# Performance work log

Measured on AMD Instinct MI355X. Metric: run time of the kernel, lower is better.

The kernel has to match this reference:

```python
import jax, jax.numpy as jnp
import numpy as np
from jax import lax

B = 256
R_ITERS = 3

def squash(x):
    # x * |x| / (1 + |x|^2), applied along last axis
    n = jnp.linalg.norm(x, axis=-1, keepdims=True)
    return x * n / (1.0 + n * n)

def conv2d(x, w, b, stride):
    y = lax.conv_general_dilated(x, w, window_strides=(stride, stride), padding='VALID',
                                 dimension_numbers=('NCHW', 'OIHW', 'NCHW'))
    return y + b[None, :, None, None]

def setup_inputs() -> dict:
    key = jax.random.key(0)
    ks = jax.random.split(key, 12)
    s = 0.05
    return {
        'x': jax.random.normal(ks[0], (B, 1, 28, 28), jnp.float32),
        'label': jax.random.randint(ks[1], (B,), 0, 10),
        'conv1_w': jax.random.normal(ks[2], (256, 1, 9, 9), jnp.float32) * s,
        'conv1_b': jnp.zeros((256,), jnp.float32),
        'pconv_w': jax.random.normal(ks[3], (256, 256, 9, 9), jnp.float32) * s,
        'pconv_b': jnp.zeros((256,), jnp.float32),
        'W_dig': jax.random.normal(ks[4], (1152, 10, 16, 8), jnp.float32),
        'dec_w1': jax.random.normal(ks[5], (512, 160), jnp.float32) * s,
        'dec_b1': jnp.zeros((512,), jnp.float32),
        'dec_w2': jax.random.normal(ks[6], (1024, 512), jnp.float32) * s,
        'dec_b2': jnp.zeros((1024,), jnp.float32),
        'dec_w3': jax.random.normal(ks[7], (784, 1024), jnp.float32) * s,
        'dec_b3': jnp.zeros((784,), jnp.float32),
    }

def reference(x, label, conv1_w, conv1_b, pconv_w, pconv_b, W_dig,
              dec_w1, dec_b1, dec_w2, dec_b2, dec_w3, dec_b3):
    # conv stem: [B,1,28,28] -> [B,256,20,20]
    h = conv2d(x, conv1_w, conv1_b, 1)
    # primary caps conv: -> [B,256,6,6] -> [B,1152,8] -> squash
    h = conv2d(h, pconv_w, pconv_b, 2)
    caps = squash(h.reshape(h.shape[0], -1, 8))
    # prediction vectors u_hat: [B, 1152, 10, 16]
    u = jnp.einsum('iond,bid->bion', W_dig, caps)
    # dynamic routing (softmax over input-capsule axis, per original code)
    b = jnp.zeros_like(u)
    for r in range(1, R_ITERS + 1):
        c = jax.nn.softmax(b, axis=1)
        s = (c * u).sum(axis=1, keepdims=True)     # [B,1,10,16]
        v = squash(s)
        if r != R_ITERS:
            b = b + (v * u).sum(axis=-1, keepdims=True)
    v = v.squeeze(1)                               # [B,10,16]
    # masked reconstruction
    one_hot = jax.nn.one_hot(label, 10, dtype=v.dtype)
    recon = (one_hot[..., None] * v).reshape(v.shape[0], 160)
    recon = jax.nn.relu(recon @ dec_w1.T + dec_b1)
    recon = jax.nn.relu(recon @ dec_w2.T + dec_b2)
    recon = jax.nn.sigmoid(recon @ dec_w3.T + dec_b3)
    return (v, recon, one_hot)
```

## Files before the change

### kernel.cpp

```cpp
#include <hip/hip_runtime.h>
#include <hip/hip_bf16.h>
#include <stdint.h>


typedef short short8 __attribute__((ext_vector_type(8)));
typedef unsigned short u16x8 __attribute__((ext_vector_type(8)));
typedef float f32x4  __attribute__((ext_vector_type(4)));

__device__ inline float bf2f(unsigned short u) {
    unsigned int v = ((unsigned int)u) << 16;
    float f;
    __builtin_memcpy(&f, &v, 4);
    return f;
}
__device__ inline unsigned short f2bf(float f) {
    __hip_bfloat16 h = __float2bfloat16(f);
    unsigned short u;
    __builtin_memcpy(&u, &h, 2);
    return u;
}
__device__ inline float clampf(float x, float b) {
    return fminf(fmaxf(x, -b), b);
}
__device__ inline float rdf(const void* p, size_t i, int f) {
    return f ? ((const float*)p)[i] : bf2f(((const unsigned short*)p)[i]);
}
__device__ inline void gload_lds16(const unsigned short* g, unsigned short* l) {
    __builtin_amdgcn_global_load_lds(
        (const __attribute__((address_space(1))) void*)g,
        (__attribute__((address_space(3))) void*)l, 16, 0, 0);
}
__device__ inline int detect_f(const void* w1c) {
    const unsigned short* w = (const unsigned short*)w1c;
    int lane = threadIdx.x & 63;
    int cnt = 0;
#pragma unroll
    for (int j = 0; j < 4; ++j) {
        float v = fabsf(bf2f(w[lane * 4 + j]));
        if (v > 100.f) cnt++;
    }
#pragma unroll
    for (int off = 32; off; off >>= 1) cnt += __shfl_xor(cnt, off);
    return cnt >= 4;
}

__global__ __launch_bounds__(256) void k_prep(
        const void* __restrict__ w1c, const void* __restrict__ w2c,
        float* __restrict__ h2f, unsigned short* __restrict__ B1p,
        unsigned short* __restrict__ Bp3) {
    __shared__ unsigned short wl[20736];
    int blk = blockIdx.x, tid = threadIdx.x;
    if (blk < 2304) {
        ((f32x4*)h2f)[blk * 256 + tid] = (f32x4){0.f, 0.f, 0.f, 0.f};
    } else if (blk < 2400) {
        int f = detect_f(w1c);
        int idx = (blk - 2304) * 256 + tid;
        int co = idx / 96, k = idx - co * 96;
        B1p[idx] = (k < 81) ? f2bf(rdf(w1c, (size_t)co * 81 + k, f)) : (unsigned short)0;
    } else {
        int f = detect_f(w1c);
        int co = blk - 2400;
        size_t base = (size_t)co * 20736;
        for (int i = tid; i < 20736; i += 256)
            wl[i] = f2bf(rdf(w2c, base + i, f));
        __syncthreads();
        for (int idx = tid; idx < 20736; idx += 256) {
            int t = idx >> 8, ci = idx & 255;
            int kc = ci >> 6, cin = ci & 63;
            Bp3[((size_t)(t * 4 + kc) << 14) + (co << 6) + cin] = wl[ci * 81 + t];
        }
    }
}

__global__ __launch_bounds__(256) void k_prep2(
        const void* __restrict__ wdig, const void* __restrict__ dw2,
        const void* __restrict__ dw3, const void* __restrict__ w1c,
        unsigned short* __restrict__ Wdb2,
        unsigned short* __restrict__ w2b,
        unsigned short* __restrict__ w3b) {
    __shared__ unsigned short wl[20480];
    int f = detect_f(w1c);
    int blk = blockIdx.x, tid = threadIdx.x;
    if (blk < 72) {
        int i0 = blk * 16;
        size_t base = (size_t)i0 * 1280;
        for (int idx = tid; idx < 20480; idx += 256)
            wl[idx] = f2bf(rdf(wdig, base + idx, f));
        __syncthreads();
        if (tid < 160) {
            int o = tid / 16, n = tid - o * 16;
            unsigned short* dst = Wdb2 + (size_t)o * 147456 + n * 9216 + i0 * 8;
            const unsigned short* src = wl + tid * 8;
#pragma unroll
            for (int i = 0; i < 16; ++i)
                *(uint4*)(dst + i * 8) = *(const uint4*)(src + i * 1280);
        }
    } else if (blk < 2120) {
        int idx = (blk - 72) * 256 + tid;
        w2b[idx] = f2bf(rdf(dw2, idx, f));
    } else {
        int idx = (blk - 2120) * 256 + tid;
        w3b[idx] = (idx < 802816) ? f2bf(rdf(dw3, idx, f)) : (unsigned short)0;
    }
}

__global__ __launch_bounds__(256) void k_conv1(
        const void* __restrict__ x,
        const unsigned short* __restrict__ B1p,
        const void* __restrict__ bias,
        unsigned short* __restrict__ h1p,
        const void* __restrict__ w1c) {
    __shared__ unsigned short xl[1568];
    __shared__ int offt[96];
    int f = detect_f(w1c);
    int tid = threadIdx.x;
    if (tid < 96) offt[tid] = (tid < 81) ? (tid / 9) * 28 + (tid % 9) : 0;

    int mblk = blockIdx.x * 128;
    int bfirst = mblk / 400;
    int blast = (mblk + 127) / 400;
    int nload = (blast - bfirst + 1) * 784;
    for (int i = tid; i < nload; i += 256)
        xl[i] = f2bf(rdf(x, (size_t)bfirst * 784 + i, f));
    __syncthreads();

    int wave = tid >> 6, lane = tid & 63;
    int wr = wave >> 1, wc = wave & 1;
    int mbase = mblk + wr * 64;
    int nbase = blockIdx.y * 128 + wc * 64;
    int l15 = lane & 15, l4 = lane >> 4;

    int lbase[4];
#pragma unroll
    for (int mt = 0; mt < 4; ++mt) {
        int m = mbase + mt * 16 + l15;
        int img = m / 400 - bfirst, pos = m % 400;
        lbase[mt] = img * 784 + (pos / 20) * 28 + (pos % 20);
    }

    f32x4 acc[4][4];
#pragma unroll
    for (int mt = 0; mt < 4; ++mt)
#pragma unroll
        for (int nt = 0; nt < 4; ++nt)
            acc[mt][nt] = (f32x4){0.f, 0.f, 0.f, 0.f};

#pragma unroll
    for (int kc = 0; kc < 3; ++kc) {
        int kbase = kc * 32 + l4 * 8;
        short8 af[4], bfr[4];
#pragma unroll
        for (int mt = 0; mt < 4; ++mt)
#pragma unroll
            for (int j = 0; j < 8; ++j) {
                int k = kbase + j;
                af[mt][j] = (k < 81) ? (short)xl[lbase[mt] + offt[k]] : (short)0;
            }
#pragma unroll
        for (int nt = 0; nt < 4; ++nt)
            bfr[nt] = *(const short8*)(B1p + (size_t)(nbase + nt * 16 + l15) * 96 + kbase);
#pragma unroll
        for (int mt = 0; mt < 4; ++mt)
#pragma unroll
            for (int nt = 0; nt < 4; ++nt)
                acc[mt][nt] = __builtin_amdgcn_mfma_f32_16x16x32_bf16(
                    af[mt], bfr[nt], acc[mt][nt], 0, 0, 0);
    }

#pragma unroll
    for (int mt = 0; mt < 4; ++mt)
#pragma unroll
        for (int nt = 0; nt < 4; ++nt) {
            int col = nbase + nt * 16 + l15;
            float bv = rdf(bias, col, f);
#pragma unroll
            for (int r = 0; r < 4; ++r) {
                int row = mbase + mt * 16 + l4 * 4 + r;
                h1p[(size_t)row * 256 + col] = f2bf(clampf(acc[mt][nt][r] + bv, 1024.f));
            }
        }
}

__global__ __launch_bounds__(256) void k_conv2(
        const unsigned short* __restrict__ h1p,
        const unsigned short* __restrict__ Bp,
        float* __restrict__ h2f) {
    __shared__ unsigned short As[3][4096];
    __shared__ unsigned short Bs[3][4096];
    int tid = threadIdx.x;
    int wave = tid >> 6, lane = tid & 63;
    int wr = wave >> 1, wc = wave & 1;

    int lin = blockIdx.x + 72 * (blockIdx.y + (blockIdx.z << 1));
    int xcd = lin & 7, sub = lin >> 3;
    int mb = ((xcd * 9) + (sub >> 4)) << 7;
    int yz = sub & 15;
    int nb = (yz & 1) << 7;
    int s = yz >> 1;
    int t0 = (81 * s) >> 3, t1 = (81 * (s + 1)) >> 3;
    int l15 = lane & 15, l4 = lane >> 4;

    int rsub = lane >> 2;
    int slog = (lane & 3) ^ ((lane >> 3) & 3);
    int aoff[2], boff[2];
#pragma unroll
    for (int r = 0; r < 2; ++r) {
        int row = wave * 32 + r * 16 + rsub;
        int m = mb + row;
        int bb = m / 36, pos = m - bb * 36;
        int y = pos / 6, xx = pos - y * 6;
        aoff[r] = (bb * 400 + y * 40 + xx * 2) * 256 + slog * 8;
        boff[r] = row * 64 + slog * 8;
    }

    int ko = (l4 ^ ((l15 >> 1) & 3)) << 3;
    int arow[4], brow[4];
#pragma unroll
    for (int mt = 0; mt < 4; ++mt) arow[mt] = ((wr * 64 + mt * 16 + l15) << 5) + ko;
#pragma unroll
    for (int nt = 0; nt < 4; ++nt) brow[nt] = ((wc * 64 + nt * 16 + l15) << 5) + ko;

    f32x4 acc[4][4];
#pragma unroll
    for (int mt = 0; mt < 4; ++mt)
#pragma unroll
        for (int nt = 0; nt < 4; ++nt)
            acc[mt][nt] = (f32x4){0.f, 0.f, 0.f, 0.f};

    int skc = 0;
    int sky = t0 / 9, skx = t0 - sky * 9;
    int stadd = (sky * 20 + skx) << 8;
    int st4 = t0 * 4;

    auto stage = [&](int buf) {
        const unsigned short* aw = h1p + stadd + (skc << 5);
        const unsigned short* bw = Bp + (((size_t)(st4 + (skc >> 1))) << 14)
                                     + nb * 64 + ((skc & 1) << 5);
        unsigned short* al = &As[buf][wave << 10];
        unsigned short* bl = &Bs[buf][wave << 10];
#pragma unroll
        for (int r = 0; r < 2; ++r) {
            gload_lds16(aw + aoff[r], al + (r << 9));
            gload_lds16(bw + boff[r], bl + (r << 9));
        }
    };
    auto adv = [&]() {
        if (++skc == 8) {
            skc = 0; st4 += 4;
            if (++skx == 9) { skx = 0; stadd += 3072; }
            else            { stadd += 256; }
        }
    };
    auto compute = [&](int buf) {
        short8 af[4], bfr[4];
#pragma unroll
        for (int mt = 0; mt < 4; ++mt)
            af[mt] = *(const short8*)(&As[buf][arow[mt]]);
#pragma unroll
        for (int nt = 0; nt < 4; ++nt)
            bfr[nt] = *(const short8*)(&Bs[buf][brow[nt]]);
#pragma unroll
        for (int mt = 0; mt < 4; ++mt)
#pragma unroll
            for (int nt = 0; nt < 4; ++nt)
                acc[mt][nt] = __builtin_amdgcn_mfma_f32_16x16x32_bf16(
                    af[mt], bfr[nt], acc[mt][nt], 0, 0, 0);
    };

    int nit = (t1 - t0) * 8;
    stage(0); adv();
    stage(1); adv();
    int cur = 0;
    for (int i = 0; i < nit; ++i) {
        if (i + 1 < nit) asm volatile("s_waitcnt vmcnt(4)" ::: "memory");
        else             asm volatile("s_waitcnt vmcnt(0)" ::: "memory");
        __builtin_amdgcn_s_barrier();
        if (i + 2 < nit) { stage(cur == 0 ? 2 : cur - 1); adv(); }
        compute(cur);
        cur = (cur == 2) ? 0 : cur + 1;
    }

#pragma unroll
    for (int mt = 0; mt < 4; ++mt)
#pragma unroll
        for (int nt = 0; nt < 4; ++nt) {
            int col = nb + wc * 64 + nt * 16 + l15;
#pragma unroll
            for (int r = 0; r < 4; ++r) {
                int row = mb + wr * 64 + mt * 16 + l4 * 4 + r;
                atomicAdd(&h2f[(size_t)row * 256 + col], acc[mt][nt][r]);
            }
        }
}

__global__ __launch_bounds__(256) void k_caps2(
        const float* __restrict__ h2f, const void* __restrict__ pb,
        unsigned short* __restrict__ caps, const void* __restrict__ w1c) {
    __shared__ float ld[9216];
    int f = detect_f(w1c);
    int b = blockIdx.x, tid = threadIdx.x;
#pragma unroll 4
    for (int p = 0; p < 36; ++p)
        ld[p * 256 + tid] = h2f[(size_t)b * 9216 + p * 256 + tid];
    __syncthreads();
    for (int c = tid; c < 1152; c += 256) {
        float h[8], ss = 0.f;
#pragma unroll
        for (int d = 0; d < 8; ++d) {
            int flat = c * 8 + d;
            int co = flat / 36, pos = flat - co * 36;
            float v = clampf(ld[pos * 256 + co] + rdf(pb, co, f), 20000.f);
            h[d] = v;
            ss += v * v;
        }
        float sc = sqrtf(ss) / (1.f + ss);
        u16x8 cv;
#pragma unroll
        for (int d = 0; d < 8; ++d) cv[d] = f2bf(h[d] * sc);
        *(u16x8*)(caps + ((size_t)b * 1152 + c) * 8) = cv;
    }
}

__global__ __launch_bounds__(384) void k_routing(
        const unsigned short* __restrict__ caps, const unsigned short* __restrict__ Wdb2,
        const int* __restrict__ label, void* __restrict__ d_out,
        float* __restrict__ vsel, const void* __restrict__ w1c) {
    int f = detect_f(w1c);
    int bo = blockIdx.x;
    int b = bo / 10, o = bo - b * 10;
    int tid = threadIdx.x;
    int wid = tid >> 6, lane = tid & 63;

    __shared__ float redw[6][16];
    __shared__ float sbuf[16];
    __shared__ float mred[8];
    __shared__ float sred[8];

    float u[3][16];
    float a[3] = {0.f, 0.f, 0.f};
    const unsigned short* capb = caps + (size_t)b * 9216;
    const unsigned short* wob = Wdb2 + (size_t)o * 147456;

#pragma unroll
    for (int r = 0; r < 3; ++r) {
        int i = tid + r * 384;
        u16x8 cq = *(const u16x8*)(capb + i * 8);
        float cf[8];
#pragma unroll
        for (int d = 0; d < 8; ++d) cf[d] = bf2f(cq[d]);
#pragma unroll
        for (int n = 0; n < 16; ++n) {
            u16x8 q = *(const u16x8*)(wob + ((size_t)n * 1152 + i) * 8);
            float sacc = 0.f;
#pragma unroll
            for (int d = 0; d < 8; ++d) sacc += bf2f(q[d]) * cf[d];
            u[r][n] = sacc;
        }
    }

    for (int rr = 1; rr <= 3; ++rr) {
        float mx = fmaxf(fmaxf(a[0], a[1]), a[2]);
#pragma unroll
        for (int off = 32; off; off >>= 1) mx = fmaxf(mx, __shfl_xor(mx, off));
        if (lane == 0) mred[wid] = mx;
        __syncthreads();
        float M = mred[0];
#pragma unroll
        for (int w = 1; w < 6; ++w) M = fmaxf(M, mred[w]);

        float e[3], es = 0.f;
#pragma unroll
        for (int r = 0; r < 3; ++r) { e[r] = __expf(a[r] - M); es += e[r]; }
#pragma unroll
        for (int off = 32; off; off >>= 1) es += __shfl_xor(es, off);
        if (lane == 0) sred[wid] = es;
        __syncthreads();
        float S = 0.f;
#pragma unroll
        for (int w = 0; w < 6; ++w) S += sred[w];
        float inv = 1.f / S;

        float p[16];
#pragma unroll
        for (int n = 0; n < 16; ++n)
            p[n] = (e[0] * u[0][n] + e[1] * u[1][n] + e[2] * u[2][n]) * inv;
#pragma unroll
        for (int n = 0; n < 16; ++n)
#pragma unroll
            for (int off = 32; off; off >>= 1) p[n] += __shfl_xor(p[n], off);
        if (lane == 0)
#pragma unroll
            for (int n = 0; n < 16; ++n) redw[wid][n] = p[n];
        __syncthreads();
        if (tid < 16) {
            float sn = 0.f;
#pragma unroll
            for (int w = 0; w < 6; ++w) sn += redw[w][tid];
            sbuf[tid] = sn;
        }
        __syncthreads();

        float ss = 0.f;
#pragma unroll
        for (int n = 0; n < 16; ++n) ss += sbuf[n] * sbuf[n];
        float sc = sqrtf(ss) / (1.f + ss);

        if (rr < 3) {
#pragma unroll
            for (int r = 0; r < 3; ++r) {
                float dot = 0.f;
#pragma unroll
                for (int n = 0; n < 16; ++n) dot += sbuf[n] * u[r][n];
                a[r] += sc * dot;
            }
            __syncthreads();
        } else {
            int lbl = label[b];
            if (tid < 16) {
                float vn = clampf(sbuf[tid] * sc, 1.f);
                if (f) ((float*)d_out)[(bo << 4) + tid] = vn;
                else   ((unsigned short*)d_out)[(bo << 4) + tid] = f2bf(vn);
                if (o == lbl) vsel[(b << 4) + tid] = vn;
            }
            if (tid == 0) {
                float oh = (o == lbl) ? 1.f : 0.f;
                if (f) ((float*)d_out)[241664 + bo] = oh;
                else   ((unsigned short*)d_out)[241664 + bo] = f2bf(oh);
            }
        }
    }
}

__global__ void k_dec1(const float* __restrict__ vsel, const int* __restrict__ label,
                       const void* __restrict__ w1, const void* __restrict__ b1,
                       unsigned short* __restrict__ r1b, const void* __restrict__ w1c) {
    int f = detect_f(w1c);
    int b = blockIdx.x, j = threadIdx.x;
    __shared__ float vs[16];
    if (j < 16) vs[j] = vsel[b * 16 + j];
    __syncthreads();
    int lbl = label[b];
    size_t wb = (size_t)j * 160 + lbl * 16;
    float acc = rdf(b1, j, f);
#pragma unroll
    for (int n = 0; n < 16; ++n) acc += rdf(w1, wb + n, f) * vs[n];
    r1b[b * 512 + j] = f2bf(fmaxf(acc, 0.f));
}

__global__ __launch_bounds__(256) void k_dgemm(
        const unsigned short* __restrict__ A, const unsigned short* __restrict__ B,
        const void* __restrict__ bias, int K, int mode, int nvalid, int ostride,
        unsigned short* __restrict__ outb, void* __restrict__ d_out,
        const void* __restrict__ w1c) {
    int f = detect_f(w1c);
    int tid = threadIdx.x;
    int wave = tid >> 6, lane = tid & 63;
    int wr = wave >> 1, wc = wave & 1;
    int mbase = blockIdx.x * 128 + wr * 64;
    int nbase = blockIdx.y * 128 + wc * 64;
    int l15 = lane & 15, l4 = lane >> 4;
    int koff = l4 * 8;

    f32x4 acc[4][4];
#pragma unroll
    for (int mt = 0; mt < 4; ++mt)
#pragma unroll
        for (int nt = 0; nt < 4; ++nt)
            acc[mt][nt] = (f32x4){0.f, 0.f, 0.f, 0.f};

    int nch = K >> 5;
    for (int kc = 0; kc < nch; ++kc) {
        int k0 = kc * 32 + koff;
        short8 af[4], bfr[4];
#pragma unroll
        for (int mt = 0; mt < 4; ++mt)
            af[mt] = *(const short8*)(A + (size_t)(mbase + mt * 16 + l15) * K + k0);
#pragma unroll
        for (int nt = 0; nt < 4; ++nt)
            bfr[nt] = *(const short8*)(B + (size_t)(nbase + nt * 16 + l15) * K + k0);
#pragma unroll
        for (int mt = 0; mt < 4; ++mt)
#pragma unroll
            for (int nt = 0; nt < 4; ++nt)
                acc[mt][nt] = __builtin_amdgcn_mfma_f32_16x16x32_bf16(
                    af[mt], bfr[nt], acc[mt][nt], 0, 0, 0);
    }

#pragma unroll
    for (int mt = 0; mt < 4; ++mt)
#pragma unroll
        for (int nt = 0; nt < 4; ++nt) {
            int col = nbase + nt * 16 + l15;
            float bv = (col < nvalid) ? rdf(bias, col, f) : 0.f;
#pragma unroll
            for (int r = 0; r < 4; ++r) {
                int row = mbase + mt * 16 + l4 * 4 + r;
                float v = acc[mt][nt][r] + bv;
                if (mode == 0) {
                    outb[(size_t)row * ostride + col] = f2bf(fmaxf(v, 0.f));
                } else if (col < nvalid) {
                    float a = clampf(v, 60.f);
                    float sig = 1.f / (1.f + __expf(-a));
                    size_t oi = 40960 + (size_t)row * 784 + col;
                    if (f) ((float*)d_out)[oi] = sig;
                    else   ((unsigned short*)d_out)[oi] = f2bf(sig);
                }
            }
        }
}

extern "C" void kernel_launch(void* const* d_in, const int* in_sizes, int n_in,
                              void* d_out, int out_size, void* d_ws, size_t ws_size,
                              hipStream_t stream) {
    const void* x    = d_in[0];
    const int*  lbl  = (const int*)d_in[1];
    const void* w1c  = d_in[2];
    const void* b1c  = d_in[3];
    const void* w2c  = d_in[4];
    const void* b2c  = d_in[5];
    const void* wdig = d_in[6];
    const void* dw1  = d_in[7];
    const void* db1  = d_in[8];
    const void* dw2  = d_in[9];
    const void* db2  = d_in[10];
    const void* dw3  = d_in[11];
    const void* db3  = d_in[12];
    (void)in_sizes; (void)n_in; (void)out_size; (void)ws_size;

    char* ws = (char*)d_ws;
    float* h2f           = (float*)(ws);
    unsigned short* Bp3  = (unsigned short*)(ws + 9437184);
    unsigned short* caps = (unsigned short*)(ws + 9437184);
    unsigned short* B1p  = (unsigned short*)(ws + 20054016);
    unsigned short* h1p  = (unsigned short*)(ws + 20103168);
    unsigned short* Wdb2 = (unsigned short*)(ws + 20103168);
    unsigned short* w2b  = (unsigned short*)(ws + 23052288);
    unsigned short* w3b  = (unsigned short*)(ws + 24100864);
    unsigned short* r1b  = (unsigned short*)(ws + 25935872);
    unsigned short* r2b  = (unsigned short*)(ws + 26198016);
    float* vsel          = (float*)(ws + 26722304);

    hipLaunchKernelGGL(k_prep,  dim3(2656),     dim3(256), 0, stream, w1c, w2c, h2f, B1p, Bp3);
    hipLaunchKernelGGL(k_conv1, dim3(800, 2),   dim3(256), 0, stream, x, B1p, b1c, h1p, w1c);
    hipLaunchKernelGGL(k_conv2, dim3(72, 2, 8), dim3(256), 0, stream, h1p, Bp3, h2f);
    hipLaunchKernelGGL(k_prep2, dim3(5704),     dim3(256), 0, stream,
                       wdig, dw2, dw3, w1c, Wdb2, w2b, w3b);
    hipLaunchKernelGGL(k_caps2, dim3(256),      dim3(256), 0, stream, h2f, b2c, caps, w1c);
    hipLaunchKernelGGL(k_routing, dim3(2560),   dim3(384), 0, stream, caps, Wdb2, lbl,
                       d_out, vsel, w1c);
    hipLaunchKernelGGL(k_dec1,  dim3(256),      dim3(512), 0, stream, vsel, lbl, dw1, db1, r1b, w1c);
    hipLaunchKernelGGL(k_dgemm, dim3(2, 8),     dim3(256), 0, stream,
                       r1b, w2b, db2, 512, 0, 1024, 1024, r2b, d_out, w1c);
    hipLaunchKernelGGL(k_dgemm, dim3(2, 7),     dim3(256), 0, stream,
                       r2b, w3b, db3, 1024, 1, 784, 0, (unsigned short*)nullptr, d_out, w1c);
}
```

Measured before the change: 552.4 us.

## Store conv1 output in stride-2 polyphase planes and simplify conv2 block mapping

The conv1 epilogue now writes h1 into four parity planes (even/odd row × even/odd column), each a dense 10x10 grid per image. With this layout the stride-2 conv2 gather reads contiguous neighbouring positions within one plane, which should improve locality for the A-tile loads. Conv2 also drops its XCD-aware swizzle of block indices in favour of a plain blockIdx mapping. That can lower L2 reuse across chiplets, and the conv1 stores become more scattered.

```diff
diff --git a/kernel.cpp b/kernel.cpp
--- a/kernel.cpp
+++ b/kernel.cpp
@@ -6,6 +6,8 @@
 typedef short short8 __attribute__((ext_vector_type(8)));
 typedef unsigned short u16x8 __attribute__((ext_vector_type(8)));
 typedef float f32x4  __attribute__((ext_vector_type(4)));
+
+#define H1_PLANE 6553600
 
 __device__ inline float bf2f(unsigned short u) {
     unsigned int v = ((unsigned int)u) << 16;
@@ -168,17 +170,25 @@
     }
 
 #pragma unroll
-    for (int mt = 0; mt < 4; ++mt)
+    for (int mt = 0; mt < 4; ++mt) {
+        size_t radr[4];
+#pragma unroll
+        for (int r = 0; r < 4; ++r) {
+            int m = mbase + mt * 16 + l4 * 4 + r;
+            int img = m / 400, pos = m - img * 400;
+            int y = pos / 20, xx = pos - y * 20;
+            radr[r] = (size_t)(((y & 1) << 1) + (xx & 1)) * H1_PLANE
+                    + (size_t)(img * 100 + (y >> 1) * 10 + (xx >> 1)) * 256;
+        }
 #pragma unroll
         for (int nt = 0; nt < 4; ++nt) {
             int col = nbase + nt * 16 + l15;
             float bv = rdf(bias, col, f);
 #pragma unroll
-            for (int r = 0; r < 4; ++r) {
-                int row = mbase + mt * 16 + l4 * 4 + r;
-                h1p[(size_t)row * 256 + col] = f2bf(clampf(acc[mt][nt][r] + bv, 1024.f));
-            }
-        }
+            for (int r = 0; r < 4; ++r)
+                h1p[radr[r] + col] = f2bf(clampf(acc[mt][nt][r] + bv, 1024.f));
+        }
+    }
 }
 
 __global__ __launch_bounds__(256) void k_conv2(
@@ -190,13 +200,9 @@
     int tid = threadIdx.x;
     int wave = tid >> 6, lane = tid & 63;
     int wr = wave >> 1, wc = wave & 1;
-
-    int lin = blockIdx.x + 72 * (blockIdx.y + (blockIdx.z << 1));
-    int xcd = lin & 7, sub = lin >> 3;
-    int mb = ((xcd * 9) + (sub >> 4)) << 7;
-    int yz = sub & 15;
-    int nb = (yz & 1) << 7;
-    int s = yz >> 1;
+    int mb = blockIdx.x << 7;
+    int nb = blockIdx.y << 7;
+    int s = blockIdx.z;
     int t0 = (81 * s) >> 3, t1 = (81 * (s + 1)) >> 3;
     int l15 = lane & 15, l4 = lane >> 4;
 
@@ -208,8 +214,8 @@
         int row = wave * 32 + r * 16 + rsub;
         int m = mb + row;
         int bb = m / 36, pos = m - bb * 36;
-        int y = pos / 6, xx = pos - y * 6;
-        aoff[r] = (bb * 400 + y * 40 + xx * 2) * 256 + slog * 8;
+        int yo = pos / 6, xo = pos - yo * 6;
+        aoff[r] = (bb * 100 + yo * 10 + xo) * 256 + slog * 8;
         boff[r] = row * 64 + slog * 8;
     }
 
@@ -229,11 +235,12 @@
 
     int skc = 0;
     int sky = t0 / 9, skx = t0 - sky * 9;
-    int stadd = (sky * 20 + skx) << 8;
     int st4 = t0 * 4;
+    int tboff = ((sky & 1) * 2 + (skx & 1)) * H1_PLANE
+              + ((sky >> 1) * 10 + (skx >> 1)) * 256;
 
     auto stage = [&](int buf) {
-        const unsigned short* aw = h1p + stadd + (skc << 5);
+        const unsigned short* aw = h1p + tboff + (skc << 5);
         const unsigned short* bw = Bp + (((size_t)(st4 + (skc >> 1))) << 14)
                                      + nb * 64 + ((skc & 1) << 5);
         unsigned short* al = &As[buf][wave << 10];
@@ -247,8 +254,9 @@
     auto adv = [&]() {
         if (++skc == 8) {
             skc = 0; st4 += 4;
-            if (++skx == 9) { skx = 0; stadd += 3072; }
-            else            { stadd += 256; }
+            if (++skx == 9) { skx = 0; ++sky; }
+            tboff = ((sky & 1) * 2 + (skx & 1)) * H1_PLANE
+                  + ((sky >> 1) * 10 + (skx >> 1)) * 256;
         }
     };
     auto compute = [&](int buf) {
```

New measurement: 567.5 us. 1.03x slower.
